# Optimization experiments

Hardware: AMD Instinct MI355X
Metric: run time of the kernel (lower is better)

The kernel has to match this reference:

```python
import jax, jax.numpy as jnp
import numpy as np

N_HEAD = 16


def setup_inputs() -> dict:
    key = jax.random.key(0)
    k0, k1, k2, k3 = jax.random.split(key, 4)
    B, T, C = 2, 2048, 1024
    scale = 0.02
    x = jax.random.normal(k0, (B, T, C), dtype=jnp.float32)
    W_attn = jax.random.normal(k1, (C, 3 * C), dtype=jnp.float32) * scale
    b_attn = jnp.zeros((3 * C,), dtype=jnp.float32)
    W_proj = jax.random.normal(k2, (C, C), dtype=jnp.float32) * scale
    b_proj = jnp.zeros((C,), dtype=jnp.float32)
    return {"x": x, "W_attn": W_attn, "b_attn": b_attn, "W_proj": W_proj, "b_proj": b_proj}


def reference(x, W_attn, b_attn, W_proj, b_proj):
    B, T, C = x.shape
    H = N_HEAD
    hd = C // H
    # fused qkv projection
    qkv = x @ W_attn + b_attn                      # [B, T, 3C]
    q, k, v = jnp.split(qkv, 3, axis=-1)
    q = q.reshape(B, T, H, hd).transpose(0, 2, 1, 3)  # [B, H, T, hd]
    k = k.reshape(B, T, H, hd).transpose(0, 2, 1, 3)
    v = v.reshape(B, T, H, hd).transpose(0, 2, 1, 3)
    # scaled dot-product attention with causal mask (past_kv=None -> seq_len == T)
    att = jnp.einsum('bhqd,bhkd->bhqk', q, k) / jnp.sqrt(jnp.float32(hd))
    causal = jnp.tril(jnp.ones((T, T), dtype=bool))  # [T, T]
    att = jnp.where(causal[None, None, :, :], att, jnp.float32(-jnp.inf))
    att = jax.nn.softmax(att, axis=-1)
    y = jnp.einsum('bhqk,bhkd->bhqd', att, v)        # [B, H, T, hd]
    y = y.transpose(0, 2, 1, 3).reshape(B, T, C)
    y = y @ W_proj + b_proj
    return (y, k, v)  # (output, present_k, present_v)
```

## Files before the change

kernel.cpp:

```cpp
#include <hip/hip_runtime.h>
#include <hip/hip_bf16.h>

typedef __bf16 bf16;
typedef __bf16 bf16x8 __attribute__((ext_vector_type(8)));
typedef float f32x4 __attribute__((ext_vector_type(4)));
typedef unsigned int u32;

#define MFMA_BF16(a, b, c) __builtin_amdgcn_mfma_f32_16x16x32_bf16((a), (b), (c), 0, 0, 0)

#define SEQ_T 2048
#define DIM_C 1024

__device__ inline void gload16(const void* g, void* l) {
  __builtin_amdgcn_global_load_lds((const __attribute__((address_space(1))) u32*)g,
                                   (__attribute__((address_space(3))) u32*)l, 16, 0, 0);
}

__device__ inline bf16x8 cvt8f(const f32x4 a, const f32x4 b) {
  bf16x8 r;
  r[0] = (bf16)a[0]; r[1] = (bf16)a[1]; r[2] = (bf16)a[2]; r[3] = (bf16)a[3];
  r[4] = (bf16)b[0]; r[5] = (bf16)b[1]; r[6] = (bf16)b[2]; r[7] = (bf16)b[3];
  return r;
}

__global__ __launch_bounds__(256) void prep_kernel(
    const float* __restrict__ x, const float* __restrict__ Wa,
    const float* __restrict__ Wp, bf16* __restrict__ xbf,
    bf16* __restrict__ wat, bf16* __restrict__ wpt) {
  const int tid = threadIdx.x;
  const int bid = blockIdx.x;
  if (bid < 2048) {
    const size_t i = ((size_t)bid * 256 + tid) * 8;
    *(bf16x8*)(xbf + i) = cvt8f(*(const f32x4*)(x + i), *(const f32x4*)(x + i + 4));
  } else if (bid < 3584) {
    const int cid = (bid - 2048) * 256 + tid;
    const int kg = cid / 3072, n = cid - kg * 3072;
    bf16x8 r;
#pragma unroll
    for (int j = 0; j < 8; j++) r[j] = (bf16)Wa[(size_t)(kg * 8 + j) * 3072 + n];
    *(bf16x8*)(wat + (size_t)cid * 8) = r;
  } else {
    const int cid = (bid - 3584) * 256 + tid;
    const int kg = cid >> 10, n = cid & 1023;
    bf16x8 r;
#pragma unroll
    for (int j = 0; j < 8; j++) r[j] = (bf16)Wp[(size_t)(kg * 8 + j) * 1024 + n];
    *(bf16x8*)(wpt + (size_t)cid * 8) = r;
  }
}

__global__ __launch_bounds__(256) void img_kernel(
    const float* __restrict__ K, const float* __restrict__ V,
    bf16* __restrict__ kimg, bf16* __restrict__ vimg, int* __restrict__ cnt) {
  const int tid = threadIdx.x;
  const int bid = blockIdx.x;
  if (bid == 0 && tid == 0) *cnt = 0;
  if (bid < 1024) {
    __shared__ bf16 vt[4096];
    const size_t tb = (size_t)bid * 4096;
    const int key = tid >> 2, cs = (tid & 3) * 16;
    const int k7 = key & 7, cq = (key >> 3) & 7;
    const float* vsrc = V + tb + (size_t)key * 64 + cs;
#pragma unroll
    for (int jj = 0; jj < 16; jj += 4) {
      const f32x4 v4 = *(const f32x4*)(vsrc + jj);
#pragma unroll
      for (int e = 0; e < 4; e++) {
        const int hr = cs + jj + e;
        vt[hr * 64 + ((cq ^ (hr & 7)) * 8) + k7] = (bf16)v4[e];
      }
    }
    __syncthreads();
    *(bf16x8*)(vimg + tb + tid * 16) = *(const bf16x8*)&vt[tid * 16];
    *(bf16x8*)(vimg + tb + tid * 16 + 8) = *(const bf16x8*)&vt[tid * 16 + 8];
  } else {
    const int gid = (bid - 1024) * 256 + tid;
    const int ka = gid >> 3, h8 = gid & 7;
    const size_t src = (size_t)ka * 64 + h8 * 8;
    const bf16x8 rk = cvt8f(*(const f32x4*)(K + src), *(const f32x4*)(K + src + 4));
    const size_t tb = (size_t)(ka & ~63) * 64;
    const int kl = ka & 63, k7 = ka & 7;
    *(bf16x8*)(kimg + tb + kl * 64 + ((h8 ^ k7) * 8)) = rk;
  }
}

template <int MODE, int BM, int BK>
__global__ __launch_bounds__(256) void gemm_kernel(
    const bf16* __restrict__ A, const bf16* __restrict__ Wt,
    const float* __restrict__ bias, float* __restrict__ out0,
    float* __restrict__ out1, bf16* __restrict__ bq, int M, int N, int K) {
  constexpr int MI = BM / 32;
  constexpr int CA = BM * BK / 2048;
  constexpr int CB = BK / 16;
  constexpr int RPC = 512 / BK;
  constexpr int EPB = BK / 8;
  __shared__ bf16 As[2][BM * BK];
  __shared__ bf16 Bt[2][128 * BK];

  const int tid = threadIdx.x;
  const int wid = tid >> 6, lane = tid & 63;
  const int quad = lane >> 4, l16 = lane & 15;
  const int wm = (wid >> 1) * (BM / 2), wn = (wid & 1) * 64;
  const int m0 = blockIdx.y * BM, n0 = blockIdx.x * 128;
  const int lr = lane / EPB, lks = lane % EPB;

  const f32x4 zero = {0.f, 0.f, 0.f, 0.f};
  f32x4 acc[MI][4];
#pragma unroll
  for (int i = 0; i < MI; i++)
#pragma unroll
    for (int j = 0; j < 4; j++) acc[i][j] = zero;

  auto stage = [&](int buf, int kk) {
#pragma unroll
    for (int p = 0; p < CA; p++) {
      const int c = wid * CA + p;
      gload16(A + (size_t)(m0 + c * RPC + lr) * K + kk + lks * 8,
              (bf16*)As[buf] + c * 512);
    }
#pragma unroll
    for (int p = 0; p < CB; p++) {
      const int c = wid * CB + p;
      gload16(Wt + ((size_t)((kk >> 3) + lks) * N + n0 + c * RPC + lr) * 8,
              (bf16*)Bt[buf] + c * 512);
    }
  };

  const int nt = K / BK;
  stage(0, 0);
  __syncthreads();
  int cur = 0;
  for (int t = 0; t < nt; t++) {
    if (t + 1 < nt) stage(cur ^ 1, (t + 1) * BK);
#pragma unroll
    for (int kb = 0; kb < BK / 32; kb++) {
      bf16x8 af[MI], bfr[4];
#pragma unroll
      for (int i = 0; i < MI; i++)
        af[i] = *(const bf16x8*)&As[cur][(wm + i * 16 + l16) * BK + kb * 32 + quad * 8];
#pragma unroll
      for (int j = 0; j < 4; j++)
        bfr[j] = *(const bf16x8*)&Bt[cur][(wn + j * 16 + l16) * BK + kb * 32 + quad * 8];
#pragma unroll
      for (int i = 0; i < MI; i++)
#pragma unroll
        for (int j = 0; j < 4; j++)
          acc[i][j] = MFMA_BF16(af[i], bfr[j], acc[i][j]);
    }
    __syncthreads();
    cur ^= 1;
  }

#pragma unroll
  for (int i = 0; i < MI; i++) {
#pragma unroll
    for (int j = 0; j < 4; j++) {
      const int col = n0 + wn + j * 16 + l16;
      const float bv = bias[col];
#pragma unroll
      for (int r = 0; r < 4; r++) {
        const int gm = m0 + wm + i * 16 + quad * 4 + r;
        const float v = acc[i][j][r] + bv;
        if (MODE == 0) {
          out0[(size_t)gm * N + col] = v;
        } else {
          const int which = col >> 10, c = col & 1023;
          const int h = c >> 6, d = c & 63;
          const int b = gm >> 11, t = gm & (SEQ_T - 1);
          const size_t idx = ((size_t)(b * 16 + h) * SEQ_T + t) * 64 + d;
          if (which == 0) {
            bq[idx] = (bf16)(v * 0.18033688f);
          } else if (which == 1) {
            out0[idx] = v;
          } else {
            out1[idx] = v;
          }
        }
      }
    }
  }
}

__global__ __launch_bounds__(512) void attn_kernel(
    const bf16* __restrict__ Qbf, const bf16* __restrict__ Kimg,
    const bf16* __restrict__ Vimg, bf16* __restrict__ Y, int* __restrict__ cnt) {
  __shared__ bf16 Ks[2][4096];
  __shared__ bf16 Vt[2][4096];
  __shared__ bf16 Ps[8 * 1024];
  __shared__ int js;

  const int tid = threadIdx.x;
  const int wid = tid >> 6, lane = tid & 63;
  const int quad = lane >> 4, l16 = lane & 15;

  bf16x8 bones;
#pragma unroll
  for (int j = 0; j < 8; j++) bones[j] = (bf16)1.0f;
  const f32x4 zero = {0.f, 0.f, 0.f, 0.f};

  for (;;) {
    if (tid == 0) js = atomicAdd(cnt, 1);
    __syncthreads();
    const int j = js;
    if (j >= 512) break;
    const int qt = 15 - (j >> 5), bh = j & 31;
    const int q0 = qt * 128;
    const int b = bh >> 4, h = bh & 15;

    const bf16* qp = Qbf + (size_t)bh * SEQ_T * 64;
    const bf16* kp = Kimg + (size_t)bh * SEQ_T * 64;
    const bf16* vp = Vimg + (size_t)bh * SEQ_T * 64;

    bf16x8 aq[2];
#pragma unroll
    for (int ks = 0; ks < 2; ks++)
      aq[ks] = *(const bf16x8*)(qp + (size_t)(q0 + wid * 16 + l16) * 64 + ks * 32 + quad * 8);

    f32x4 oacc[4], lacc;
    lacc = zero;
#pragma unroll
    for (int t = 0; t < 4; t++) oacc[t] = zero;

    const int last = 2 * qt + 1;

    auto stage = [&](int buf, int t) {
      const size_t tb = (size_t)t * 4096 + (size_t)tid * 8;
      gload16(kp + tb, &Ks[buf][wid << 9]);
      gload16(vp + tb, &Vt[buf][wid << 9]);
    };

    stage(0, 0);
    __syncthreads();

    for (int it = 0; it <= last; ++it) {
      const int cur = it & 1;
      if (it < last) stage(cur ^ 1, it + 1);

      const bool skip = (it == last) && (wid < 4);
      const bool dm = (it == 2 * qt && wid < 4) || (it == last && wid >= 4);

      if (!skip) {
        f32x4 sa[4];
#pragma unroll
        for (int nt = 0; nt < 4; nt++) {
          const int row = nt * 16 + l16, r7 = l16 & 7;
          const bf16x8 bk0 = *(const bf16x8*)&Ks[cur][row * 64 + ((quad ^ r7) * 8)];
          const bf16x8 bk1 = *(const bf16x8*)&Ks[cur][row * 64 + (((quad + 4) ^ r7) * 8)];
          f32x4 s = MFMA_BF16(aq[0], bk0, zero);
          sa[nt] = MFMA_BF16(aq[1], bk1, s);
        }
        if (dm) {
#pragma unroll
          for (int nt = 0; nt < 4; nt++) {
            const int col = it * 64 + nt * 16 + l16;
#pragma unroll
            for (int r = 0; r < 4; r++) {
              const int row = q0 + wid * 16 + quad * 4 + r;
              if (col > row) sa[nt][r] = -1e30f;
            }
          }
        }
        bf16* pwb = &Ps[wid * 1024];
#pragma unroll
        for (int nt = 0; nt < 4; nt++) {
#pragma unroll
          for (int r = 0; r < 4; r++) {
            const int pr = quad * 4 + r;
            pwb[pr * 64 + (((2 * nt + (l16 >> 3)) ^ (pr & 7)) * 8) + (l16 & 7)] =
                (bf16)exp2f(sa[nt][r]);
          }
        }
        bf16x8 ap[2];
#pragma unroll
        for (int ks = 0; ks < 2; ks++)
          ap[ks] = *(const bf16x8*)&pwb[l16 * 64 + (((ks * 4 + quad) ^ (l16 & 7)) * 8)];
        lacc = MFMA_BF16(ap[0], bones, lacc);
        lacc = MFMA_BF16(ap[1], bones, lacc);
#pragma unroll
        for (int nt = 0; nt < 4; nt++) {
          const int hr = nt * 16 + l16, h7 = l16 & 7;
#pragma unroll
          for (int ks = 0; ks < 2; ks++) {
            const bf16x8 bv = *(const bf16x8*)&Vt[cur][hr * 64 + (((ks * 4 + quad) ^ h7) * 8)];
            oacc[nt] = MFMA_BF16(ap[ks], bv, oacc[nt]);
          }
        }
      }
      __syncthreads();
    }

    float inv[4];
#pragma unroll
    for (int r = 0; r < 4; r++) inv[r] = 1.f / lacc[r];
#pragma unroll
    for (int nt = 0; nt < 4; nt++) {
#pragma unroll
      for (int r = 0; r < 4; r++) {
        const int row = q0 + wid * 16 + quad * 4 + r;
        const int col = h * 64 + nt * 16 + l16;
        Y[((size_t)(b * SEQ_T + row)) * DIM_C + col] = (bf16)(oacc[nt][r] * inv[r]);
      }
    }
  }
}

extern "C" void kernel_launch(void* const* d_in, const int* in_sizes, int n_in,
                              void* d_out, int out_size, void* d_ws, size_t ws_size,
                              hipStream_t stream) {
  (void)in_sizes; (void)n_in; (void)out_size; (void)ws_size;
  const float* x = (const float*)d_in[0];
  const float* W_attn = (const float*)d_in[1];
  const float* b_attn = (const float*)d_in[2];
  const float* W_proj = (const float*)d_in[3];
  const float* b_proj = (const float*)d_in[4];

  float* out = (float*)d_out;
  float* y_out = out;
  float* k_out = out + (size_t)4194304;
  float* v_out = out + (size_t)8388608;
  bf16* qbf = (bf16*)d_out;
  bf16* kimg = (bf16*)d_out + 4194304;
  bf16* y_att = (bf16*)d_in[0];
  bf16* vimg = (bf16*)d_in[0] + 4194304;
  bf16* xbf = (bf16*)d_ws;
  bf16* wat = xbf + 4194304;
  bf16* wpt = wat + 3145728;
  int* cnt = (int*)d_ws;

  prep_kernel<<<4096, 256, 0, stream>>>(x, W_attn, W_proj, xbf, wat, wpt);
  gemm_kernel<1, 128, 32><<<dim3(3072 / 128, 4096 / 128), 256, 0, stream>>>(
      xbf, wat, b_attn, k_out, v_out, qbf, 4096, 3072, 1024);
  img_kernel<<<3072, 256, 0, stream>>>(k_out, v_out, kimg, vimg, cnt);
  attn_kernel<<<768, 512, 0, stream>>>(qbf, kimg, vimg, y_att, cnt);
  gemm_kernel<0, 64, 64><<<dim3(1024 / 128, 4096 / 64), 256, 0, stream>>>(
      y_att, wpt, b_proj, y_out, nullptr, nullptr, 4096, 1024, 1024);
}
```

Before: 211.9 us.

## Replace persistent atomic scheduler with static grid and double-size KV stages

The attention kernel drops its persistent atomic work queue and becomes a static 16x32 grid. Each block takes one query tile, with tile order reversed for the first 16 heads to balance causal work. Each pipeline stage now loads 128 keys instead of 64, which halves the barriers and loop iterations per tile at the cost of twice the LDS for K and V. This may reduce occupancy and gives up the dynamic load balancing the atomic counter provided.

```diff
diff --git a/kernel.cpp b/kernel.cpp
--- a/kernel.cpp
+++ b/kernel.cpp
@@ -51,10 +51,9 @@
 
 __global__ __launch_bounds__(256) void img_kernel(
     const float* __restrict__ K, const float* __restrict__ V,
-    bf16* __restrict__ kimg, bf16* __restrict__ vimg, int* __restrict__ cnt) {
+    bf16* __restrict__ kimg, bf16* __restrict__ vimg) {
   const int tid = threadIdx.x;
   const int bid = blockIdx.x;
-  if (bid == 0 && tid == 0) *cnt = 0;
   if (bid < 1024) {
     __shared__ bf16 vt[4096];
     const size_t tb = (size_t)bid * 4096;
@@ -183,123 +182,125 @@
 
 __global__ __launch_bounds__(512) void attn_kernel(
     const bf16* __restrict__ Qbf, const bf16* __restrict__ Kimg,
-    const bf16* __restrict__ Vimg, bf16* __restrict__ Y, int* __restrict__ cnt) {
-  __shared__ bf16 Ks[2][4096];
-  __shared__ bf16 Vt[2][4096];
+    const bf16* __restrict__ Vimg, bf16* __restrict__ Y) {
+  __shared__ bf16 Ks[2][8192];
+  __shared__ bf16 Vt[2][8192];
   __shared__ bf16 Ps[8 * 1024];
-  __shared__ int js;
 
   const int tid = threadIdx.x;
   const int wid = tid >> 6, lane = tid & 63;
   const int quad = lane >> 4, l16 = lane & 15;
 
+  const int qt = (blockIdx.y < 16) ? ((int)gridDim.x - 1 - (int)blockIdx.x)
+                                   : (int)blockIdx.x;
+  const int bh = blockIdx.y;
+  const int q0 = qt * 128;
+  const int b = bh >> 4, h = bh & 15;
+
+  const bf16* qp = Qbf + (size_t)bh * SEQ_T * 64;
+  const bf16* kp = Kimg + (size_t)bh * SEQ_T * 64;
+  const bf16* vp = Vimg + (size_t)bh * SEQ_T * 64;
+
+  bf16x8 aq[2];
+#pragma unroll
+  for (int ks = 0; ks < 2; ks++)
+    aq[ks] = *(const bf16x8*)(qp + (size_t)(q0 + wid * 16 + l16) * 64 + ks * 32 + quad * 8);
+
   bf16x8 bones;
 #pragma unroll
   for (int j = 0; j < 8; j++) bones[j] = (bf16)1.0f;
+
   const f32x4 zero = {0.f, 0.f, 0.f, 0.f};
-
-  for (;;) {
-    if (tid == 0) js = atomicAdd(cnt, 1);
-    __syncthreads();
-    const int j = js;
-    if (j >= 512) break;
-    const int qt = 15 - (j >> 5), bh = j & 31;
-    const int q0 = qt * 128;
-    const int b = bh >> 4, h = bh & 15;
-
-    const bf16* qp = Qbf + (size_t)bh * SEQ_T * 64;
-    const bf16* kp = Kimg + (size_t)bh * SEQ_T * 64;
-    const bf16* vp = Vimg + (size_t)bh * SEQ_T * 64;
-
-    bf16x8 aq[2];
-#pragma unroll
-    for (int ks = 0; ks < 2; ks++)
-      aq[ks] = *(const bf16x8*)(qp + (size_t)(q0 + wid * 16 + l16) * 64 + ks * 32 + quad * 8);
-
-    f32x4 oacc[4], lacc;
-    lacc = zero;
-#pragma unroll
-    for (int t = 0; t < 4; t++) oacc[t] = zero;
-
-    const int last = 2 * qt + 1;
-
-    auto stage = [&](int buf, int t) {
-      const size_t tb = (size_t)t * 4096 + (size_t)tid * 8;
-      gload16(kp + tb, &Ks[buf][wid << 9]);
-      gload16(vp + tb, &Vt[buf][wid << 9]);
-    };
-
-    stage(0, 0);
-    __syncthreads();
-
-    for (int it = 0; it <= last; ++it) {
-      const int cur = it & 1;
-      if (it < last) stage(cur ^ 1, it + 1);
-
-      const bool skip = (it == last) && (wid < 4);
-      const bool dm = (it == 2 * qt && wid < 4) || (it == last && wid >= 4);
-
-      if (!skip) {
-        f32x4 sa[4];
+  f32x4 oacc[4], lacc;
+  lacc = zero;
+#pragma unroll
+  for (int t = 0; t < 4; t++) oacc[t] = zero;
+
+  const int lastg = 2 * qt + 1;
+
+  auto stage = [&](int buf, int itt) {
+    const size_t tb = (size_t)itt * 8192 + (size_t)tid * 8;
+    gload16(kp + tb, &Ks[buf][wid << 9]);
+    gload16(kp + tb + 4096, &Ks[buf][4096 + (wid << 9)]);
+    gload16(vp + tb, &Vt[buf][wid << 9]);
+    gload16(vp + tb + 4096, &Vt[buf][4096 + (wid << 9)]);
+  };
+
+  stage(0, 0);
+  __syncthreads();
+
+  for (int it = 0; it <= qt; ++it) {
+    const int cur = it & 1;
+    if (it < qt) stage(cur ^ 1, it + 1);
+
+#pragma unroll
+    for (int s = 0; s < 2; s++) {
+      const int g = 2 * it + s;
+      const bool skip = (g == lastg) && (wid < 4);
+      const bool dm = (g == 2 * qt && wid < 4) || (g == lastg && wid >= 4);
+      if (skip) continue;
+      const bf16* ksb = &Ks[cur][s * 4096];
+      const bf16* vtb = &Vt[cur][s * 4096];
+
+      f32x4 sa[4];
+#pragma unroll
+      for (int nt = 0; nt < 4; nt++) {
+        const int row = nt * 16 + l16, r7 = l16 & 7;
+        const bf16x8 bk0 = *(const bf16x8*)&ksb[row * 64 + ((quad ^ r7) * 8)];
+        const bf16x8 bk1 = *(const bf16x8*)&ksb[row * 64 + (((quad + 4) ^ r7) * 8)];
+        f32x4 sacc = MFMA_BF16(aq[0], bk0, zero);
+        sa[nt] = MFMA_BF16(aq[1], bk1, sacc);
+      }
+      if (dm) {
 #pragma unroll
         for (int nt = 0; nt < 4; nt++) {
-          const int row = nt * 16 + l16, r7 = l16 & 7;
-          const bf16x8 bk0 = *(const bf16x8*)&Ks[cur][row * 64 + ((quad ^ r7) * 8)];
-          const bf16x8 bk1 = *(const bf16x8*)&Ks[cur][row * 64 + (((quad + 4) ^ r7) * 8)];
-          f32x4 s = MFMA_BF16(aq[0], bk0, zero);
-          sa[nt] = MFMA_BF16(aq[1], bk1, s);
-        }
-        if (dm) {
-#pragma unroll
-          for (int nt = 0; nt < 4; nt++) {
-            const int col = it * 64 + nt * 16 + l16;
-#pragma unroll
-            for (int r = 0; r < 4; r++) {
-              const int row = q0 + wid * 16 + quad * 4 + r;
-              if (col > row) sa[nt][r] = -1e30f;
-            }
+          const int col = g * 64 + nt * 16 + l16;
+#pragma unroll
+          for (int r = 0; r < 4; r++) {
+            const int row = q0 + wid * 16 + quad * 4 + r;
+            if (col > row) sa[nt][r] = -1e30f;
           }
         }
-        bf16* pwb = &Ps[wid * 1024];
-#pragma unroll
-        for (int nt = 0; nt < 4; nt++) {
-#pragma unroll
-          for (int r = 0; r < 4; r++) {
-            const int pr = quad * 4 + r;
-            pwb[pr * 64 + (((2 * nt + (l16 >> 3)) ^ (pr & 7)) * 8) + (l16 & 7)] =
-                (bf16)exp2f(sa[nt][r]);
-          }
+      }
+      bf16* pwb = &Ps[wid * 1024];
+#pragma unroll
+      for (int nt = 0; nt < 4; nt++) {
+#pragma unroll
+        for (int r = 0; r < 4; r++) {
+          const int pr = quad * 4 + r;
+          pwb[pr * 64 + (((2 * nt + (l16 >> 3)) ^ (pr & 7)) * 8) + (l16 & 7)] =
+              (bf16)exp2f(sa[nt][r]);
         }
-        bf16x8 ap[2];
-#pragma unroll
-        for (int ks = 0; ks < 2; ks++)
-          ap[ks] = *(const bf16x8*)&pwb[l16 * 64 + (((ks * 4 + quad) ^ (l16 & 7)) * 8)];
-        lacc = MFMA_BF16(ap[0], bones, lacc);
-        lacc = MFMA_BF16(ap[1], bones, lacc);
-#pragma unroll
-        for (int nt = 0; nt < 4; nt++) {
-          const int hr = nt * 16 + l16, h7 = l16 & 7;
-#pragma unroll
-          for (int ks = 0; ks < 2; ks++) {
-            const bf16x8 bv = *(const bf16x8*)&Vt[cur][hr * 64 + (((ks * 4 + quad) ^ h7) * 8)];
-            oacc[nt] = MFMA_BF16(ap[ks], bv, oacc[nt]);
-          }
+      }
+      bf16x8 ap[2];
+#pragma unroll
+      for (int ks = 0; ks < 2; ks++)
+        ap[ks] = *(const bf16x8*)&pwb[l16 * 64 + (((ks * 4 + quad) ^ (l16 & 7)) * 8)];
+      lacc = MFMA_BF16(ap[0], bones, lacc);
+      lacc = MFMA_BF16(ap[1], bones, lacc);
+#pragma unroll
+      for (int nt = 0; nt < 4; nt++) {
+        const int hr = nt * 16 + l16, h7 = l16 & 7;
+#pragma unroll
+        for (int ks = 0; ks < 2; ks++) {
+          const bf16x8 bv = *(const bf16x8*)&vtb[hr * 64 + (((ks * 4 + quad) ^ h7) * 8)];
+          oacc[nt] = MFMA_BF16(ap[ks], bv, oacc[nt]);
         }
       }
-      __syncthreads();
-    }
-
-    float inv[4];
-#pragma unroll
-    for (int r = 0; r < 4; r++) inv[r] = 1.f / lacc[r];
-#pragma unroll
-    for (int nt = 0; nt < 4; nt++) {
-#pragma unroll
-      for (int r = 0; r < 4; r++) {
-        const int row = q0 + wid * 16 + quad * 4 + r;
-        const int col = h * 64 + nt * 16 + l16;
-        Y[((size_t)(b * SEQ_T + row)) * DIM_C + col] = (bf16)(oacc[nt][r] * inv[r]);
-      }
+    }
+    __syncthreads();
+  }
+
+  float inv[4];
+#pragma unroll
+  for (int r = 0; r < 4; r++) inv[r] = 1.f / lacc[r];
+#pragma unroll
+  for (int nt = 0; nt < 4; nt++) {
+#pragma unroll
+    for (int r = 0; r < 4; r++) {
+      const int row = q0 + wid * 16 + quad * 4 + r;
+      const int col = h * 64 + nt * 16 + l16;
+      Y[((size_t)(b * SEQ_T + row)) * DIM_C + col] = (bf16)(oacc[nt][r] * inv[r]);
     }
   }
 }
@@ -325,13 +326,12 @@
   bf16* xbf = (bf16*)d_ws;
   bf16* wat = xbf + 4194304;
   bf16* wpt = wat + 3145728;
-  int* cnt = (int*)d_ws;
 
   prep_kernel<<<4096, 256, 0, stream>>>(x, W_attn, W_proj, xbf, wat, wpt);
   gemm_kernel<1, 128, 32><<<dim3(3072 / 128, 4096 / 128), 256, 0, stream>>>(
       xbf, wat, b_attn, k_out, v_out, qbf, 4096, 3072, 1024);
-  img_kernel<<<3072, 256, 0, stream>>>(k_out, v_out, kimg, vimg, cnt);
-  attn_kernel<<<768, 512, 0, stream>>>(qbf, kimg, vimg, y_att, cnt);
+  img_kernel<<<3072, 256, 0, stream>>>(k_out, v_out, kimg, vimg);
+  attn_kernel<<<dim3(16, 32), 512, 0, stream>>>(qbf, kimg, vimg, y_att);
   gemm_kernel<0, 64, 64><<<dim3(1024 / 128, 4096 / 64), 256, 0, stream>>>(
       y_att, wpt, b_proj, y_out, nullptr, nullptr, 4096, 1024, 1024);
 }
```

Result: faster. 202.1 us (-4.6%).
